# Performance work log

Measured on AMD Instinct MI355X. Metric: run time of the kernel, lower is better.

Reference implementation:

```python
import jax, jax.numpy as jnp
import numpy as np

N_QUBITS = 10
N_LAYERS = 3
BATCH = 16384
PI = 3.14159265358979


def _cnot_perm(c, t, n):
    # Basis-state permutation for CNOT(control=c, target=t); wire 0 = MSB.
    k = np.arange(1 << n)
    cbit = (k >> (n - 1 - c)) & 1
    perm = np.where(cbit == 1, k ^ (1 << (n - 1 - t)), k)
    return jnp.asarray(perm, dtype=jnp.int32)


def _ry_mat(a):
    # a: [...] angles -> [..., 2, 2] real rotation, cast to complex64
    h = a * 0.5
    c, s = jnp.cos(h), jnp.sin(h)
    U = jnp.stack([jnp.stack([c, -s], -1), jnp.stack([s, c], -1)], -2)
    return U.astype(jnp.complex64)


def _rx_mat(a):
    h = a * 0.5
    c, s = jnp.cos(h).astype(jnp.complex64), jnp.sin(h).astype(jnp.complex64)
    mis = -1j * s
    return jnp.stack([jnp.stack([c, mis], -1), jnp.stack([mis, c], -1)], -2)


def _apply_1q(state, U, q, n):
    # state: [B, 2^n]; U: [2,2] (shared) or [B,2,2] (per-sample)
    L, R = 1 << q, 1 << (n - 1 - q)
    s = state.reshape(-1, L, 2, R)
    if U.ndim == 3:
        s = jnp.einsum('bij,bljr->blir', U, s)
    else:
        s = jnp.einsum('ij,bljr->blir', U, s)
    return s.reshape(-1, 1 << n)


def _apply_rz(state, a, q, n):
    # shared scalar angle a; diagonal phase gate
    L, R = 1 << q, 1 << (n - 1 - q)
    h = a * 0.5
    ph = jnp.exp(1j * jnp.stack([-h, h]).astype(jnp.complex64))  # [2]
    s = state.reshape(-1, L, 2, R) * ph[None, None, :, None]
    return s.reshape(-1, 1 << n)


def _z_signs(n):
    k = np.arange(1 << n)
    signs = np.stack([1.0 - 2.0 * ((k >> (n - 1 - w)) & 1) for w in range(n)])
    return jnp.asarray(signs, dtype=jnp.float32)  # [n, 2^n]


def setup_inputs() -> dict:
    key = jax.random.key(0)
    kx, kw = jax.random.split(key)
    x = jax.random.normal(kx, (BATCH, N_QUBITS), dtype=jnp.float32)
    weights = jax.random.normal(kw, (N_LAYERS, N_QUBITS, 3), dtype=jnp.float32) * 0.1
    return {"x": x, "weights": weights}


def reference(x, weights):
    B, n = x.shape
    n_layers = weights.shape[0]
    enc = jnp.tanh(x) * PI  # pre-scaled angle encoding, [B, n]

    state = jnp.zeros((B, 1 << n), dtype=jnp.complex64).at[:, 0].set(1.0)

    # RY angle encoding (batched gates)
    for q in range(n):
        state = _apply_1q(state, _ry_mat(enc[:, q]), q, n)

    perms = [_cnot_perm(i, (i + 1) % n, n) for i in range(n)]
    for layer in range(n_layers):
        for i in range(n):
            state = state[:, perms[i]]  # CNOT ring
        for i in range(n):
            state = _apply_1q(state, _rx_mat(weights[layer, i, 0]), i, n)
            state = _apply_1q(state, _ry_mat(weights[layer, i, 1]), i, n)
            state = _apply_rz(state, weights[layer, i, 2], i, n)

    probs = state.real ** 2 + state.imag ** 2  # [B, 2^n]
    return probs @ _z_signs(n).T  # [B, n] PauliZ expectations
```

## Files before the change

kernel.cpp:

```cpp
#include <hip/hip_runtime.h>
#include <math.h>

#define NQ 10
#define NL 3
#define PI_F 3.14159265358979f
#define TPB 256

typedef _Float16 f16x8 __attribute__((ext_vector_type(8)));
typedef _Float16 h2t  __attribute__((ext_vector_type(2)));
typedef float    f32x4 __attribute__((ext_vector_type(4)));

__host__ __device__ constexpr int cnot_chain_ce(int j) {
    for (int i = NQ - 1; i >= 0; --i) {
        int tq = (i + 1) % NQ;
        j ^= ((j >> (NQ - 1 - i)) & 1) << (NQ - 1 - tq);
    }
    return j;
}

__device__ __forceinline__ unsigned pkh(float r, float i) {
    return __builtin_bit_cast(unsigned, __builtin_amdgcn_cvt_pkrtz(r, i));
}

__device__ __forceinline__ f16x8 mkfrag(unsigned d0, unsigned d1, unsigned d2,
                                        unsigned d3, unsigned d4, unsigned d5,
                                        unsigned d6, unsigned d7, unsigned sel) {
    uint4 u;
    u.x = __builtin_amdgcn_perm(d1, d0, sel);
    u.y = __builtin_amdgcn_perm(d3, d2, sel);
    u.z = __builtin_amdgcn_perm(d5, d4, sel);
    u.w = __builtin_amdgcn_perm(d7, d6, sel);
    return __builtin_bit_cast(f16x8, u);
}

template<int MASK>
__device__ __forceinline__ unsigned lxu(unsigned v) {
    if constexpr (MASK == 1)
        return (unsigned)__builtin_amdgcn_update_dpp(0, (int)v, 0xB1, 0xF, 0xF, true);
    else if constexpr (MASK == 2)
        return (unsigned)__builtin_amdgcn_update_dpp(0, (int)v, 0x4E, 0xF, 0xF, true);
    else if constexpr (MASK == 4) {
        int a = __builtin_amdgcn_update_dpp(0, (int)v, 0x1B, 0xF, 0xF, true);
        return (unsigned)__builtin_amdgcn_update_dpp(0, a, 0x141, 0xF, 0xF, true);
    } else if constexpr (MASK == 8) {
        int a = __builtin_amdgcn_update_dpp(0, (int)v, 0x141, 0xF, 0xF, true);
        return (unsigned)__builtin_amdgcn_update_dpp(0, a, 0x140, 0xF, 0xF, true);
    } else if constexpr (MASK == 16)
        return (unsigned)__builtin_amdgcn_ds_swizzle((int)v, 0x401F);
    else
        return (unsigned)__shfl_xor((int)v, 32, 64);
}
#define WR1(v, M) v += __builtin_bit_cast(float, lxu<M>(__builtin_bit_cast(unsigned, v)));
#define WRED(v) { WR1(v,1) WR1(v,2) WR1(v,4) WR1(v,8) WR1(v,16) WR1(v,32) }

#define FORALL16(F) F(0) F(1) F(2) F(3) F(4) F(5) F(6) F(7) \
                    F(8) F(9) F(10) F(11) F(12) F(13) F(14) F(15)
#define FORALLQ(F) F(0) F(1) F(2) F(3) F(4) F(5) F(6) F(7) F(8) F(9)

__global__ void vq_prep(const float* __restrict__ w, uint4* __restrict__ frag,
                        float* __restrict__ qcoef) {
    __shared__ float msh[NL * NQ][8];
    const int tid = threadIdx.x;
    if (tid < NL * NQ) {
        const float* wp = w + tid * 3;
        float sa = __sinf(wp[0]*0.5f), ca = __cosf(wp[0]*0.5f);
        float sb = __sinf(wp[1]*0.5f), cb = __cosf(wp[1]*0.5f);
        float sc = __sinf(wp[2]*0.5f), cc = __cosf(wp[2]*0.5f);
        float c00r = cb*ca,  c00i =  sa*sb;
        float c01r = -sb*ca, c01i = -cb*sa;
        float c10r =  sb*ca, c10i = -cb*sa;
        float c11r =  cb*ca, c11i = -sb*sa;
        float m[8];
        m[0] = cc*c00r + sc*c00i;  m[1] = cc*c00i - sc*c00r;
        m[2] = cc*c01r + sc*c01i;  m[3] = cc*c01i - sc*c01r;
        m[4] = cc*c10r - sc*c10i;  m[5] = cc*c10i + sc*c10r;
        m[6] = cc*c11r - sc*c11i;  m[7] = cc*c11i + sc*c11r;
#pragma unroll
        for (int j = 0; j < 8; ++j) msh[tid][j] = m[j];
        const int l = tid / NQ, q = tid % NQ;
        if (q < 2)
#pragma unroll
            for (int j = 0; j < 8; ++j) qcoef[(l*2 + q)*8 + j] = m[j];
    }
    __syncthreads();
    const int lane = tid & 63, wg = tid >> 6;
    const int mrow = lane & 15, quad = lane >> 4;
#pragma unroll 1
    for (int c = 0; c < 3; ++c) {
        const int id = c*4 + wg;
        const int l = id >> 2, s = (id >> 1) & 1, v = id & 1;
        const int qb = s ? 2 : 6;
        unsigned pd[4];
#pragma unroll
        for (int d = 0; d < 4; ++d) {
            float hv[2];
#pragma unroll
            for (int h = 0; h < 2; ++h) {
                const int k = quad*8 + 2*d + h;
                const int col = k & 15;
                float er = 1.f, ei = 0.f;
#pragma unroll
                for (int p = 0; p < 4; ++p) {
                    const float* mm = msh[l*NQ + qb + p];
                    const int rb = (mrow >> (3-p)) & 1, cb2 = (col >> (3-p)) & 1;
                    const float gr = mm[(rb*2 + cb2)*2], gi = mm[(rb*2 + cb2)*2 + 1];
                    const float nr = er*gr - ei*gi, ni = er*gi + ei*gr;
                    er = nr; ei = ni;
                }
                hv[h] = (k < 16) ? (v ? ei : er) : (v ? er : -ei);
            }
            h2t hh; hh.x = (_Float16)hv[0]; hh.y = (_Float16)hv[1];
            pd[d] = __builtin_bit_cast(unsigned, hh);
        }
        frag[id*64 + lane] = make_uint4(pd[0], pd[1], pd[2], pd[3]);
    }
}


#define DECLF(q) float f0_##q, f1_##q;
#define MKF(q) { float e_ = __expf(2.0f * xr[q]); \
    float h_ = (1.0f - 2.0f / (e_ + 1.0f)) * (PI_F * 0.5f); \
    f1_##q = __sinf(h_); f0_##q = __cosf(h_); }

#define IST(J) { float a_ = pr \
    * ((((J) >> 3) & 1) ? f1_6 : f0_6) * ((((J) >> 2) & 1) ? f1_7 : f0_7) \
    * ((((J) >> 1) & 1) ? f1_8 : f0_8) * (((J) & 1) ? f1_9 : f0_9); \
    P[17*lane + (J)] = pkh(a_, 0.0f); }

#define LDA1(b,i) { constexpr int pc_ = cnot_chain_ce((b)*256) ^ cnot_chain_ce(i); \
    const int pk_ = PBv ^ pc_; dw##i = P[pk_ + (pk_ >> 4)]; }
#define GATH(b) LDA1(b,0) LDA1(b,1) LDA1(b,2) LDA1(b,3) LDA1(b,4) LDA1(b,5) LDA1(b,6) LDA1(b,7) \
    fr##b = mkfrag(dw0,dw1,dw2,dw3,dw4,dw5,dw6,dw7,psel);

#define LDB1(b,i) dw##i = P[sB + 272*(b) + 17*(i)];
#define GATB(b) LDB1(b,0) LDB1(b,1) LDB1(b,2) LDB1(b,3) LDB1(b,4) LDB1(b,5) LDB1(b,6) LDB1(b,7) \
    fr##b = mkfrag(dw0,dw1,dw2,dw3,dw4,dw5,dw6,dw7,psel);

#define MMA_A(b) { \
    f32x4 cr_ = __builtin_amdgcn_mfma_f32_16x16x32_f16(aAr, fr##b, z4, 0, 0, 0); \
    f32x4 ci_ = __builtin_amdgcn_mfma_f32_16x16x32_f16(aAi, fr##b, z4, 0, 0, 0); \
    P[sAst + 272*(b)    ] = pkh(cr_.x, ci_.x); \
    P[sAst + 272*(b) + 1] = pkh(cr_.y, ci_.y); \
    P[sAst + 272*(b) + 2] = pkh(cr_.z, ci_.z); \
    P[sAst + 272*(b) + 3] = pkh(cr_.w, ci_.w); }

#define MMA_B(b) \
    car##b = __builtin_amdgcn_mfma_f32_16x16x32_f16(aBr, fr##b, z4, 0, 0, 0); \
    cai##b = __builtin_amdgcn_mfma_f32_16x16x32_f16(aBi, fr##b, z4, 0, 0, 0);

#define CGATE(pa, pb, qp) { \
    const float g0_=(qp)[0], g1_=(qp)[1], g2_=(qp)[2], g3_=(qp)[3]; \
    const float g4_=(qp)[4], g5_=(qp)[5], g6_=(qp)[6], g7_=(qp)[7]; \
    f32x4 ar_ = car##pa, ai_ = cai##pa, br_ = car##pb, bi_ = cai##pb; \
    car##pa = g0_*ar_ - g1_*ai_ + g2_*br_ - g3_*bi_; \
    cai##pa = g0_*ai_ + g1_*ar_ + g2_*bi_ + g3_*br_; \
    car##pb = g4_*ar_ - g5_*ai_ + g6_*br_ - g7_*bi_; \
    cai##pb = g4_*ai_ + g5_*ar_ + g6_*bi_ + g7_*br_; }

#define STL(b) { P[sBst + 272*(b)     ] = pkh(car##b.x, cai##b.x); \
                 P[sBst + 272*(b) + 17] = pkh(car##b.y, cai##b.y); \
                 P[sBst + 272*(b) + 34] = pkh(car##b.z, cai##b.z); \
                 P[sBst + 272*(b) + 51] = pkh(car##b.w, cai##b.w); }

#define ROD(b, r, comp) { const float p_ = car##b.comp*car##b.comp + cai##b.comp*cai##b.comp; \
    Sx += p_; \
    aq0 += ((b)&2) ? -p_ : p_;  aq1 += ((b)&1) ? -p_ : p_; \
    aq4 += ((r)&2) ? -p_ : p_;  aq5 += ((r)&1) ? -p_ : p_; }
#define ROB(b) ROD(b,0,x) ROD(b,1,y) ROD(b,2,z) ROD(b,3,w)

__global__ __launch_bounds__(TPB)
__attribute__((amdgpu_waves_per_eu(4, 4)))
void vq_main(const float* __restrict__ x, const uint4* __restrict__ frag,
             const float* __restrict__ qcoef, float* __restrict__ out) {
    __shared__ unsigned pl[4][1088];
    const int tid = threadIdx.x, wv = tid >> 6, lane = tid & 63;
    unsigned* P = pl[wv];
    const int elem = __builtin_amdgcn_readfirstlane(blockIdx.x * 4 + wv);
    const int n = lane & 15, quad = lane >> 4;
    const unsigned psel = (lane & 32) ? 0x07060302u : 0x05040100u;

    int Pn = 0;
#pragma unroll
    for (int mm = 0; mm < 4; ++mm)
        Pn ^= ((n >> mm) & 1) ? cnot_chain_ce(16 << mm) : 0;
    const int PBv = Pn ^ ((quad & 1) ? cnot_chain_ce(8) : 0);
    const int sB   = n + 17 * ((quad & 1) * 8);
    const int sAst = 17*n + 4*quad;
    const int sBst = 68*quad + n;

    const float* xr = x + elem * NQ;
    FORALLQ(DECLF)
    FORALLQ(MKF)
    {
        const float pr = (((lane>>5)&1) ? f1_0 : f0_0) * (((lane>>4)&1) ? f1_1 : f0_1)
                       * (((lane>>3)&1) ? f1_2 : f0_2) * (((lane>>2)&1) ? f1_3 : f0_3)
                       * (((lane>>1)&1) ? f1_4 : f0_4) * ((lane&1) ? f1_5 : f0_5);
        FORALL16(IST)
    }

    f32x4 car0, car1, car2, car3, cai0, cai1, cai2, cai3;
    const f32x4 z4 = {0.f, 0.f, 0.f, 0.f};

#pragma unroll 1
    for (int l = 0; l < NL; ++l) {
        const uint4* fp = frag + l*4*64;
        const f16x8 aAr = __builtin_bit_cast(f16x8, fp[lane]);
        const f16x8 aAi = __builtin_bit_cast(f16x8, fp[64 + lane]);
        const f16x8 aBr = __builtin_bit_cast(f16x8, fp[128 + lane]);
        const f16x8 aBi = __builtin_bit_cast(f16x8, fp[192 + lane]);
        const float* qc = qcoef + l*16;
        unsigned dw0, dw1, dw2, dw3, dw4, dw5, dw6, dw7;
        f16x8 fr0, fr1, fr2, fr3;

        GATH(0) GATH(1) GATH(2) GATH(3)
        __builtin_amdgcn_wave_barrier();
        MMA_A(0) MMA_A(1) MMA_A(2) MMA_A(3)
        __builtin_amdgcn_wave_barrier();

        GATB(0) GATB(1) GATB(2) GATB(3)
        __builtin_amdgcn_wave_barrier();
        MMA_B(0) MMA_B(1) MMA_B(2) MMA_B(3)
        CGATE(0, 1, qc + 8)  CGATE(2, 3, qc + 8)
        CGATE(0, 2, qc)      CGATE(1, 3, qc)
        if (l < NL - 1) { STL(0) STL(1) STL(2) STL(3) }
    }

    float Sx = 0.f, aq0 = 0.f, aq1 = 0.f, aq4 = 0.f, aq5 = 0.f;
    ROB(0) ROB(1) ROB(2) ROB(3)
    float w2 = ((lane>>5)&1) ? -Sx : Sx;
    float w3 = ((lane>>4)&1) ? -Sx : Sx;
    float w6 = ((lane>>3)&1) ? -Sx : Sx;
    float w7 = ((lane>>2)&1) ? -Sx : Sx;
    float w8 = ((lane>>1)&1) ? -Sx : Sx;
    float w9 = (lane&1) ? -Sx : Sx;
    WRED(aq0) WRED(aq1) WRED(w2) WRED(w3) WRED(aq4)
    WRED(aq5) WRED(w6) WRED(w7) WRED(w8) WRED(w9)
    if (lane == 0) {
        float* op = out + elem * NQ;
        op[0] = aq0; op[1] = aq1; op[2] = w2; op[3] = w3; op[4] = aq4;
        op[5] = aq5; op[6] = w6; op[7] = w7; op[8] = w8; op[9] = w9;
    }
}

extern "C" void kernel_launch(void* const* d_in, const int* in_sizes, int n_in,
                              void* d_out, int out_size, void* d_ws, size_t ws_size,
                              hipStream_t stream) {
    const float* x = (const float*)d_in[0];
    const float* w = (const float*)d_in[1];
    float* out = (float*)d_out;
    uint4* frag = (uint4*)d_ws;
    float* qcoef = (float*)((char*)d_ws + 768 * sizeof(uint4));
    const int B = in_sizes[0] / NQ;
    vq_prep<<<dim3(1), dim3(TPB), 0, stream>>>(w, frag, qcoef);
    vq_main<<<dim3(B / 4), dim3(TPB), 0, stream>>>(x, frag, qcoef, out);
}
```

Baseline: 104.9 us.

## Re-layout intermediate LDS state for contiguous B-gather and use explicit lgkmcnt fences

Changes where the MFMA-A results are stored in the per-wave LDS scratch so the second-stage gather reads eight consecutive words per lane instead of strided ones. This lets the compiler merge those reads into wide ds_read instructions. The wave_barrier calls are replaced with explicit s_waitcnt lgkmcnt(0) fences, and an extra fence is added after initialization and after the inter-layer store. The fences force every LDS operation to drain, which may reduce latency overlap, and the new layout could add bank conflicts on the strided stores.

```diff
diff --git a/kernel.cpp b/kernel.cpp
--- a/kernel.cpp
+++ b/kernel.cpp
@@ -9,6 +9,8 @@
 typedef _Float16 f16x8 __attribute__((ext_vector_type(8)));
 typedef _Float16 h2t  __attribute__((ext_vector_type(2)));
 typedef float    f32x4 __attribute__((ext_vector_type(4)));
+
+#define LDSFENCE asm volatile("s_waitcnt lgkmcnt(0)" ::: "memory")
 
 __host__ __device__ constexpr int cnot_chain_ce(int j) {
     for (int i = NQ - 1; i >= 0; --i) {
@@ -132,17 +134,18 @@
 #define GATH(b) LDA1(b,0) LDA1(b,1) LDA1(b,2) LDA1(b,3) LDA1(b,4) LDA1(b,5) LDA1(b,6) LDA1(b,7) \
     fr##b = mkfrag(dw0,dw1,dw2,dw3,dw4,dw5,dw6,dw7,psel);
 
-#define LDB1(b,i) dw##i = P[sB + 272*(b) + 17*(i)];
-#define GATB(b) LDB1(b,0) LDB1(b,1) LDB1(b,2) LDB1(b,3) LDB1(b,4) LDB1(b,5) LDB1(b,6) LDB1(b,7) \
-    fr##b = mkfrag(dw0,dw1,dw2,dw3,dw4,dw5,dw6,dw7,psel);
-
 #define MMA_A(b) { \
     f32x4 cr_ = __builtin_amdgcn_mfma_f32_16x16x32_f16(aAr, fr##b, z4, 0, 0, 0); \
     f32x4 ci_ = __builtin_amdgcn_mfma_f32_16x16x32_f16(aAi, fr##b, z4, 0, 0, 0); \
-    P[sAst + 272*(b)    ] = pkh(cr_.x, ci_.x); \
-    P[sAst + 272*(b) + 1] = pkh(cr_.y, ci_.y); \
-    P[sAst + 272*(b) + 2] = pkh(cr_.z, ci_.z); \
-    P[sAst + 272*(b) + 3] = pkh(cr_.w, ci_.w); }
+    P[sA + 16*(b)      ] = pkh(cr_.x, ci_.x); \
+    P[sA + 16*(b) +  68] = pkh(cr_.y, ci_.y); \
+    P[sA + 16*(b) + 136] = pkh(cr_.z, ci_.z); \
+    P[sA + 16*(b) + 204] = pkh(cr_.w, ci_.w); }
+
+#define GATB(b) { const int gb_ = 68*n + 8*q1 + 16*(b); \
+    dw0 = P[gb_    ]; dw1 = P[gb_ + 1]; dw2 = P[gb_ + 2]; dw3 = P[gb_ + 3]; \
+    dw4 = P[gb_ + 4]; dw5 = P[gb_ + 5]; dw6 = P[gb_ + 6]; dw7 = P[gb_ + 7]; \
+    fr##b = mkfrag(dw0,dw1,dw2,dw3,dw4,dw5,dw6,dw7,psel); }
 
 #define MMA_B(b) \
     car##b = __builtin_amdgcn_mfma_f32_16x16x32_f16(aBr, fr##b, z4, 0, 0, 0); \
@@ -172,20 +175,19 @@
 __attribute__((amdgpu_waves_per_eu(4, 4)))
 void vq_main(const float* __restrict__ x, const uint4* __restrict__ frag,
              const float* __restrict__ qcoef, float* __restrict__ out) {
-    __shared__ unsigned pl[4][1088];
+    __shared__ __align__(16) unsigned pl[4][1088];
     const int tid = threadIdx.x, wv = tid >> 6, lane = tid & 63;
     unsigned* P = pl[wv];
     const int elem = __builtin_amdgcn_readfirstlane(blockIdx.x * 4 + wv);
-    const int n = lane & 15, quad = lane >> 4;
+    const int n = lane & 15, quad = lane >> 4, q1 = quad & 1;
     const unsigned psel = (lane & 32) ? 0x07060302u : 0x05040100u;
 
     int Pn = 0;
 #pragma unroll
     for (int mm = 0; mm < 4; ++mm)
         Pn ^= ((n >> mm) & 1) ? cnot_chain_ce(16 << mm) : 0;
-    const int PBv = Pn ^ ((quad & 1) ? cnot_chain_ce(8) : 0);
-    const int sB   = n + 17 * ((quad & 1) * 8);
-    const int sAst = 17*n + 4*quad;
+    const int PBv = Pn ^ (q1 ? cnot_chain_ce(8) : 0);
+    const int sA   = 272*quad + n;
     const int sBst = 68*quad + n;
 
     const float* xr = x + elem * NQ;
@@ -197,6 +199,7 @@
                        * (((lane>>1)&1) ? f1_4 : f0_4) * ((lane&1) ? f1_5 : f0_5);
         FORALL16(IST)
     }
+    LDSFENCE;
 
     f32x4 car0, car1, car2, car3, cai0, cai1, cai2, cai3;
     const f32x4 z4 = {0.f, 0.f, 0.f, 0.f};
@@ -213,16 +216,19 @@
         f16x8 fr0, fr1, fr2, fr3;
 
         GATH(0) GATH(1) GATH(2) GATH(3)
-        __builtin_amdgcn_wave_barrier();
+        LDSFENCE;
         MMA_A(0) MMA_A(1) MMA_A(2) MMA_A(3)
-        __builtin_amdgcn_wave_barrier();
+        LDSFENCE;
 
         GATB(0) GATB(1) GATB(2) GATB(3)
-        __builtin_amdgcn_wave_barrier();
+        LDSFENCE;
         MMA_B(0) MMA_B(1) MMA_B(2) MMA_B(3)
         CGATE(0, 1, qc + 8)  CGATE(2, 3, qc + 8)
         CGATE(0, 2, qc)      CGATE(1, 3, qc)
-        if (l < NL - 1) { STL(0) STL(1) STL(2) STL(3) }
+        if (l < NL - 1) {
+            STL(0) STL(1) STL(2) STL(3)
+            LDSFENCE;
+        }
     }
 
     float Sx = 0.f, aq0 = 0.f, aq1 = 0.f, aq4 = 0.f, aq5 = 0.f;
```

Result: faster. 99.87 us (-4.8%).
